# Optimization experiments

Hardware: AMD Instinct MI355X
Metric: run time of the kernel (lower is better)

The kernel has to match this reference:

```python
import jax, jax.numpy as jnp
import numpy as np

NUM_EXPERTS = 8
IN_FEATURES = 2048
OUT_FEATURES = 2048
TOTAL_TOKENS = 16384


def setup_inputs() -> dict:
    key = jax.random.key(0)
    kx, kc, kw, kb = jax.random.split(key, 4)
    X = jax.random.normal(kx, (TOTAL_TOKENS, IN_FEATURES), dtype=jnp.float32)
    # expert_offset: [E+1] monotonically increasing segment boundaries,
    # offset[0] = 0, offset[E] = TOTAL_TOKENS (tokens pre-sorted by expert).
    cuts = jnp.sort(jax.random.randint(kc, (NUM_EXPERTS - 1,), 0, TOTAL_TOKENS))
    expert_offset = jnp.concatenate([
        jnp.zeros((1,), dtype=jnp.int64),
        cuts.astype(jnp.int64),
        jnp.full((1,), TOTAL_TOKENS, dtype=jnp.int64),
    ])
    weight = jax.random.normal(kw, (NUM_EXPERTS, OUT_FEATURES, IN_FEATURES), dtype=jnp.float32) * 0.02
    bias = jax.random.normal(kb, (NUM_EXPERTS, OUT_FEATURES), dtype=jnp.float32) * 0.02
    return {"X": X, "expert_offset": expert_offset, "weight": weight, "bias": bias}


def reference(X, expert_offset, weight, bias):
    # X: [T, in], weight: [E, out, in], bias: [E, out]
    T = X.shape[0]
    E = weight.shape[0]
    # token t belongs to expert e iff offset[e] <= t < offset[e+1]
    eid = jnp.searchsorted(expert_offset[1:], jnp.arange(T), side="right")  # [T]
    Y = bias[eid]  # [T, out] per-token expert bias
    # grouped GEMM expressed as E masked dense GEMMs (E is a small fixed constant)
    for e in range(E):
        mask = (eid == e).astype(X.dtype)[:, None]  # [T, 1]
        Y = Y + mask * (X @ weight[e].T)
    return Y
```

## Files before the change

### kernel.cpp

```cpp
#include <hip/hip_runtime.h>


typedef __attribute__((ext_vector_type(8))) short s16x8;
typedef __attribute__((ext_vector_type(4))) short s16x4;
typedef __attribute__((ext_vector_type(4))) float f32x4;

typedef __attribute__((address_space(1))) void gv_t;
typedef __attribute__((address_space(3))) void lv_t;

#define BM 128
#define BN 128
#define BK 32

#define FBM 128
#define FBN 128
#define FBK 32
#define LDK 40

__device__ __forceinline__ short f2bf(float f) {
    union { float f; unsigned u; } v; v.f = f;
    unsigned r = v.u + 0x7FFFu + ((v.u >> 16) & 1u);
    return (short)(r >> 16);
}

__device__ __forceinline__ long long load_off(const void* p, int i, bool i64) {
    if (i64) return ((const long long*)p)[i];
    return (long long)((const int*)p)[i];
}

__global__ __launch_bounds__(256)
void cvt_kernel(const float* __restrict__ src, short* __restrict__ dst, long long n8) {
    long long stride = (long long)gridDim.x * 256;
    for (long long i = (long long)blockIdx.x * 256 + threadIdx.x; i < n8; i += stride) {
        float4 a = ((const float4*)src)[2 * i];
        float4 b = ((const float4*)src)[2 * i + 1];
        s16x8 o;
        o[0] = f2bf(a.x); o[1] = f2bf(a.y); o[2] = f2bf(a.z); o[3] = f2bf(a.w);
        o[4] = f2bf(b.x); o[5] = f2bf(b.y); o[6] = f2bf(b.z); o[7] = f2bf(b.w);
        ((s16x8*)dst)[i] = o;
    }
}

__device__ __forceinline__ bool sched_tile(const void* offp, bool off_i64, int NEXP,
                                           int slot, int bm,
                                           int& e_out, long long& row0, int& rows) {
    int acc_t = 0;
    for (int e = 0; e < NEXP; ++e) {
        long long s = load_off(offp, e, off_i64);
        long long t = load_off(offp, e + 1, off_i64);
        int n = (int)(t - s);
        int nt = (n + bm - 1) / bm;
        if (slot < acc_t + nt) {
            int lt = slot - acc_t;
            row0 = s + (long long)lt * bm;
            rows = (int)(t - row0);
            if (rows > bm) rows = bm;
            e_out = e;
            return true;
        }
        acc_t += nt;
    }
    return false;
}

__global__ __launch_bounds__(256)
void moe_gemm_bf16(const short* __restrict__ Xb16,
                   const void* __restrict__ offp,
                   const short* __restrict__ Wb16,
                   const float* __restrict__ Bias,
                   float* __restrict__ Y,
                   int IN_F, int OUT_F, int NEXP, int Ttot) {
    const bool off_i64 = (((const int*)offp)[NEXP] != Ttot);

    const int gx = gridDim.x, gy = gridDim.y;
    const int nwg = gx * gy;
    const int hw = blockIdx.x + gx * blockIdx.y;
    const int q = nwg >> 3, r = nwg & 7;
    const int xcd = hw & 7, lid = hw >> 3;
    const int work = (xcd < r ? xcd * (q + 1) : r * (q + 1) + (xcd - r) * q) + lid;
    const int wx = work / gy;
    const int wy = work % gy;

    int e_found; long long row0; int rows;
    if (!sched_tile(offp, off_i64, NEXP, wy, BM, e_found, row0, rows)) return;

    const int n0 = wx * BN;
    const int tid = threadIdx.x;
    const int wave = tid >> 6;
    const int lane = tid & 63;
    const int wm = (wave & 1) * 64;
    const int wn = (wave >> 1) * 64;
    const int lrow = lane & 15;
    const int kg = lane >> 4;
    const int swr = (lrow >> 1) & 3;

    __shared__ __align__(16) short As[BM * BK];
    __shared__ __align__(16) short Bs[BN * BK];

    const short* Xb = Xb16 + (size_t)row0 * IN_F;
    const short* Wb = Wb16 + (size_t)e_found * OUT_F * IN_F + (size_t)n0 * IN_F;

    const int lr4 = lane >> 2;
    const int colOff = ((lane & 3) ^ ((lr4 >> 1) & 3)) * 8;
    const int rbase = wave * 16 + lr4;
    const int ra0 = rbase;
    const int ra1 = 64 + rbase;
    const int ra0c = ra0 < rows ? ra0 : rows - 1;
    const int ra1c = ra1 < rows ? ra1 : rows - 1;

    const short* srcA0 = Xb + (size_t)ra0c * IN_F + colOff;
    const short* srcA1 = Xb + (size_t)ra1c * IN_F + colOff;
    const short* srcB0 = Wb + (size_t)rbase * IN_F + colOff;
    const short* srcB1 = Wb + (size_t)(64 + rbase) * IN_F + colOff;
    const int dA0 = wave * 512;
    const int dA1 = 2048 + wave * 512;
    const int dB0 = wave * 512;
    const int dB1 = 2048 + wave * 512;

    f32x4 acc[4][4] = {};

    for (int k0 = 0; k0 < IN_F; k0 += BK) {
        __syncthreads();
        __builtin_amdgcn_global_load_lds((gv_t*)(srcA0 + k0), (lv_t*)(As + dA0), 16, 0, 0);
        __builtin_amdgcn_global_load_lds((gv_t*)(srcA1 + k0), (lv_t*)(As + dA1), 16, 0, 0);
        __builtin_amdgcn_global_load_lds((gv_t*)(srcB0 + k0), (lv_t*)(Bs + dB0), 16, 0, 0);
        __builtin_amdgcn_global_load_lds((gv_t*)(srcB1 + k0), (lv_t*)(Bs + dB1), 16, 0, 0);
        __syncthreads();

        s16x8 af[4], bf[4];
        #pragma unroll
        for (int i = 0; i < 4; ++i)
            af[i] = *(const s16x8*)&As[(wm + i * 16 + lrow) * BK + ((kg ^ swr) * 8)];
        #pragma unroll
        for (int j = 0; j < 4; ++j)
            bf[j] = *(const s16x8*)&Bs[(wn + j * 16 + lrow) * BK + ((kg ^ swr) * 8)];

        #pragma unroll
        for (int i = 0; i < 4; ++i)
            #pragma unroll
            for (int j = 0; j < 4; ++j)
                acc[i][j] = __builtin_amdgcn_mfma_f32_16x16x32_bf16(
                    af[i], bf[j], acc[i][j], 0, 0, 0);
    }

    float bv[4];
    #pragma unroll
    for (int j = 0; j < 4; ++j)
        bv[j] = Bias[(size_t)e_found * OUT_F + n0 + wn + j * 16 + lrow];

    #pragma unroll
    for (int i = 0; i < 4; ++i) {
        #pragma unroll
        for (int r2 = 0; r2 < 4; ++r2) {
            int rr = wm + i * 16 + kg * 4 + r2;
            if (rr < rows) {
                float* yrow = Y + (size_t)(row0 + rr) * OUT_F + n0;
                #pragma unroll
                for (int j = 0; j < 4; ++j)
                    yrow[wn + j * 16 + lrow] = acc[i][j][r2] + bv[j];
            }
        }
    }
}

__global__ __launch_bounds__(256, 2)
void moe_gemm_f32(const float* __restrict__ X,
                  const void* __restrict__ offp,
                  const float* __restrict__ W,
                  const float* __restrict__ Bias,
                  float* __restrict__ Y,
                  int IN_F, int OUT_F, int NEXP, int Ttot) {
    const bool off_i64 = (((const int*)offp)[NEXP] != Ttot);
    int e_found; long long row0; int rows;
    if (!sched_tile(offp, off_i64, NEXP, blockIdx.y, FBM, e_found, row0, rows)) return;

    const int n0 = blockIdx.x * FBN;
    const int tid = threadIdx.x;
    const int wave = tid >> 6;
    const int lane = tid & 63;
    const int wm = (wave & 1) * 64;
    const int wn = (wave >> 1) * 64;
    const int lrow = lane & 15;
    const int kg = lane >> 4;

    __shared__ __align__(16) short As[FBM][LDK];
    __shared__ __align__(16) short Bs[FBN][LDK];

    const float* Xb = X + (size_t)row0 * IN_F;
    const float* Wb = W + (size_t)e_found * OUT_F * IN_F + (size_t)n0 * IN_F;

    f32x4 acc[4][4] = {};

    for (int k0 = 0; k0 < IN_F; k0 += FBK) {
        __syncthreads();
        #pragma unroll
        for (int p = 0; p < 4; ++p) {
            int idx = p * 256 + tid;
            int r = idx >> 3;
            int kc = (idx & 7) << 2;
            float4 v = make_float4(0.f, 0.f, 0.f, 0.f);
            if (r < rows) v = *(const float4*)(Xb + (size_t)r * IN_F + k0 + kc);
            s16x4 b;
            b.x = f2bf(v.x); b.y = f2bf(v.y); b.z = f2bf(v.z); b.w = f2bf(v.w);
            *(s16x4*)&As[r][kc] = b;
        }
        #pragma unroll
        for (int p = 0; p < 4; ++p) {
            int idx = p * 256 + tid;
            int r = idx >> 3;
            int kc = (idx & 7) << 2;
            float4 v = *(const float4*)(Wb + (size_t)r * IN_F + k0 + kc);
            s16x4 b;
            b.x = f2bf(v.x); b.y = f2bf(v.y); b.z = f2bf(v.z); b.w = f2bf(v.w);
            *(s16x4*)&Bs[r][kc] = b;
        }
        __syncthreads();

        s16x8 af[4], bf[4];
        #pragma unroll
        for (int i = 0; i < 4; ++i)
            af[i] = *(const s16x8*)&As[wm + i * 16 + lrow][kg * 8];
        #pragma unroll
        for (int j = 0; j < 4; ++j)
            bf[j] = *(const s16x8*)&Bs[wn + j * 16 + lrow][kg * 8];

        #pragma unroll
        for (int i = 0; i < 4; ++i)
            #pragma unroll
            for (int j = 0; j < 4; ++j)
                acc[i][j] = __builtin_amdgcn_mfma_f32_16x16x32_bf16(
                    af[i], bf[j], acc[i][j], 0, 0, 0);
    }

    float bv[4];
    #pragma unroll
    for (int j = 0; j < 4; ++j)
        bv[j] = Bias[(size_t)e_found * OUT_F + n0 + wn + j * 16 + lrow];

    #pragma unroll
    for (int i = 0; i < 4; ++i) {
        #pragma unroll
        for (int r2 = 0; r2 < 4; ++r2) {
            int rr = wm + i * 16 + kg * 4 + r2;
            if (rr < rows) {
                float* yrow = Y + (size_t)(row0 + rr) * OUT_F + n0;
                #pragma unroll
                for (int j = 0; j < 4; ++j)
                    yrow[wn + j * 16 + lrow] = acc[i][j][r2] + bv[j];
            }
        }
    }
}

extern "C" void kernel_launch(void* const* d_in, const int* in_sizes, int n_in,
                              void* d_out, int out_size, void* d_ws, size_t ws_size,
                              hipStream_t stream) {
    const float* X = (const float*)d_in[0];
    const void* off = d_in[1];
    const float* W = (const float*)d_in[2];
    const float* Bias = (const float*)d_in[3];
    float* Y = (float*)d_out;

    const int NEXP1 = in_sizes[1];
    const int NEXP = NEXP1 - 1;
    const int OUT_F = in_sizes[3] / NEXP;
    const int IN_F = (int)((long long)in_sizes[2] / NEXP / OUT_F);
    const int T = in_sizes[0] / IN_F;

    const long long Xn = (long long)T * IN_F;
    const long long Wn = (long long)NEXP * OUT_F * IN_F;
    const size_t need = (size_t)(Xn + Wn) * sizeof(short);

    const bool shape_ok = (OUT_F % BN == 0) && (IN_F % BK == 0) &&
                          (Xn % 8 == 0) && (Wn % 8 == 0);

    if (shape_ok && ws_size >= need) {
        short* wsX = (short*)d_ws;
        short* wsW = wsX + Xn;
        {
            long long n8 = Xn / 8;
            int blks = (int)((n8 + 255) / 256); if (blks > 2048) blks = 2048;
            cvt_kernel<<<blks, 256, 0, stream>>>(X, wsX, n8);
        }
        {
            long long n8 = Wn / 8;
            int blks = (int)((n8 + 255) / 256); if (blks > 2048) blks = 2048;
            cvt_kernel<<<blks, 256, 0, stream>>>(W, wsW, n8);
        }
        const int maxRowTiles = T / BM + NEXP;
        dim3 grid(OUT_F / BN, maxRowTiles);
        moe_gemm_bf16<<<grid, 256, 0, stream>>>(wsX, off, wsW, Bias, Y,
                                                IN_F, OUT_F, NEXP, T);
    } else {
        const int maxRowTiles = T / FBM + NEXP;
        dim3 grid(OUT_F / FBN, maxRowTiles);
        moe_gemm_f32<<<grid, 256, 0, stream>>>(X, off, W, Bias, Y,
                                               IN_F, OUT_F, NEXP, T);
    }
}
```

Measured before the change: 529.5 us.

## Triple-buffer LDS tiles with async global_load_lds prefetch two stages ahead

Replaces the single-buffered K loop, which did a load, barrier and compute on every step, with a three-slot LDS ring. Tile kt+2 is prefetched while tile kt is computed, and each step ends with a partial vmcnt wait plus s_barrier. The aim is to hide global load latency behind MFMA work and drop one barrier per iteration. The cost is three times the LDS use, which may cut occupancy, and reliance on hand-written waitcnt and barrier ordering being correct.

```diff
diff --git a/kernel.cpp b/kernel.cpp
--- a/kernel.cpp
+++ b/kernel.cpp
@@ -11,6 +11,7 @@
 #define BM 128
 #define BN 128
 #define BK 32
+#define SLOT (BM * BK)
 
 #define FBM 128
 #define FBN 128
@@ -94,8 +95,8 @@
     const int kg = lane >> 4;
     const int swr = (lrow >> 1) & 3;
 
-    __shared__ __align__(16) short As[BM * BK];
-    __shared__ __align__(16) short Bs[BN * BK];
+    __shared__ __align__(16) short As[3 * SLOT];
+    __shared__ __align__(16) short Bs[3 * SLOT];
 
     const short* Xb = Xb16 + (size_t)row0 * IN_F;
     const short* Wb = Wb16 + (size_t)e_found * OUT_F * IN_F + (size_t)n0 * IN_F;
@@ -117,23 +118,47 @@
     const int dB0 = wave * 512;
     const int dB1 = 2048 + wave * 512;
 
+    const int nkt = IN_F / BK;
+
+    auto STAGE = [&](int kt_, int slot_) {
+        const int k0_ = kt_ * BK;
+        __builtin_amdgcn_global_load_lds((gv_t*)(srcA0 + k0_),
+                                         (lv_t*)(As + slot_ * SLOT + dA0), 16, 0, 0);
+        __builtin_amdgcn_global_load_lds((gv_t*)(srcA1 + k0_),
+                                         (lv_t*)(As + slot_ * SLOT + dA1), 16, 0, 0);
+        __builtin_amdgcn_global_load_lds((gv_t*)(srcB0 + k0_),
+                                         (lv_t*)(Bs + slot_ * SLOT + dB0), 16, 0, 0);
+        __builtin_amdgcn_global_load_lds((gv_t*)(srcB1 + k0_),
+                                         (lv_t*)(Bs + slot_ * SLOT + dB1), 16, 0, 0);
+    };
+
+    STAGE(0, 0);
+    if (nkt > 1) {
+        STAGE(1, 1);
+        asm volatile("s_waitcnt vmcnt(4)" ::: "memory");
+    } else {
+        asm volatile("s_waitcnt vmcnt(0)" ::: "memory");
+    }
+    asm volatile("s_barrier" ::: "memory");
+
     f32x4 acc[4][4] = {};
 
-    for (int k0 = 0; k0 < IN_F; k0 += BK) {
-        __syncthreads();
-        __builtin_amdgcn_global_load_lds((gv_t*)(srcA0 + k0), (lv_t*)(As + dA0), 16, 0, 0);
-        __builtin_amdgcn_global_load_lds((gv_t*)(srcA1 + k0), (lv_t*)(As + dA1), 16, 0, 0);
-        __builtin_amdgcn_global_load_lds((gv_t*)(srcB0 + k0), (lv_t*)(Bs + dB0), 16, 0, 0);
-        __builtin_amdgcn_global_load_lds((gv_t*)(srcB1 + k0), (lv_t*)(Bs + dB1), 16, 0, 0);
-        __syncthreads();
-
+    int sc = 0;
+    for (int kt = 0; kt < nkt; ++kt) {
+        if (kt + 2 < nkt) {
+            const int sp = (sc >= 1) ? sc - 1 : 2;
+            STAGE(kt + 2, sp);
+        }
+
+        const short* aS = As + sc * SLOT;
+        const short* bS = Bs + sc * SLOT;
         s16x8 af[4], bf[4];
         #pragma unroll
         for (int i = 0; i < 4; ++i)
-            af[i] = *(const s16x8*)&As[(wm + i * 16 + lrow) * BK + ((kg ^ swr) * 8)];
+            af[i] = *(const s16x8*)&aS[(wm + i * 16 + lrow) * BK + ((kg ^ swr) * 8)];
         #pragma unroll
         for (int j = 0; j < 4; ++j)
-            bf[j] = *(const s16x8*)&Bs[(wn + j * 16 + lrow) * BK + ((kg ^ swr) * 8)];
+            bf[j] = *(const s16x8*)&bS[(wn + j * 16 + lrow) * BK + ((kg ^ swr) * 8)];
 
         #pragma unroll
         for (int i = 0; i < 4; ++i)
@@ -141,6 +166,13 @@
             for (int j = 0; j < 4; ++j)
                 acc[i][j] = __builtin_amdgcn_mfma_f32_16x16x32_bf16(
                     af[i], bf[j], acc[i][j], 0, 0, 0);
+
+        if (kt + 1 < nkt) {
+            if (kt + 2 < nkt) asm volatile("s_waitcnt vmcnt(4)" ::: "memory");
+            else              asm volatile("s_waitcnt vmcnt(0)" ::: "memory");
+            asm volatile("s_barrier" ::: "memory");
+        }
+        sc = (sc >= 2) ? 0 : sc + 1;
     }
 
     float bv[4];
```

Result: no change. 523.2 us (-1.2%).
